# Performance work log

Hardware: AMD Instinct MI355X
Metric: run time of the kernel (lower is better)

## Reference

```python
import jax, jax.numpy as jnp
import numpy as np
from jax import lax

STRIDE = 4
RADII = (0.1, 0.2)
NSAMPLES = (16, 32)


def fps(xyz, npoint):
    """Iterative farthest point sampling. xyz: (B,N,3) -> idx (B,npoint) int32."""
    B, N, _ = xyz.shape

    def body(carry, _):
        dists, last = carry  # (B,N), (B,)
        last_pt = jnp.take_along_axis(xyz, last[:, None, None], axis=1)  # (B,1,3)
        d = jnp.sum((xyz - last_pt) ** 2, axis=-1)  # (B,N)
        dists = jnp.minimum(dists, d)
        nxt = jnp.argmax(dists, axis=-1).astype(jnp.int32)
        return (dists, nxt), last

    init = (jnp.full((B, N), 1e10, xyz.dtype), jnp.zeros((B,), jnp.int32))
    _, idxs = lax.scan(body, init, None, length=npoint)
    return jnp.transpose(idxs)  # (B, npoint)


def ball_query(radius, nsample, support_xyz, query_xyz):
    """First-nsample-in-ball neighbor indices, padded with the first valid index.
    Returns idx (B,S,K) int32."""
    N = support_xyz.shape[1]
    d2 = (jnp.sum(query_xyz ** 2, -1, keepdims=True)
          + jnp.sum(support_xyz ** 2, -1)[:, None, :]
          - 2.0 * jnp.einsum('bsd,bnd->bsn', query_xyz, support_xyz))  # (B,S,N)
    in_ball = d2 <= radius * radius
    key = jnp.where(in_ball, jnp.arange(N, dtype=jnp.int32), N)  # smallest index first
    neg_key, idx = lax.top_k(-key, nsample)  # smallest keys
    valid = (-neg_key) < N
    idx = jnp.where(valid, idx, idx[..., :1])  # pad empty slots with first neighbor
    return idx


def gather_points(pts, idx):
    """pts (B,N,D), idx (B,S,K) -> (B,S,K,D)"""
    B, S, K = idx.shape
    D = pts.shape[-1]
    out = jnp.take_along_axis(pts, idx.reshape(B, S * K, 1), axis=1)
    return out.reshape(B, S, K, D)


def scale_block(query_xyz, support_xyz, feats_t, radius, nsample, weights):
    idx = ball_query(radius, nsample, support_xyz, query_xyz)
    g_xyz = gather_points(support_xyz, idx) - query_xyz[:, :, None, :]  # relative coords
    g_feat = gather_points(feats_t, idx)
    h = jnp.concatenate([g_xyz, g_feat], axis=-1)  # (B,S,K,3+C)
    for W, b in weights:  # shared pointwise MLP (1x1 conv) + ReLU
        h = jax.nn.relu(jnp.einsum('bskc,cd->bskd', h, W) + b)
    return jnp.max(h, axis=2)  # max-pool over neighbors -> (B,S,Cout)


def setup_inputs() -> dict:
    key = jax.random.key(0)
    ks = jax.random.split(key, 10)
    B, N, C = 8, 8192, 64
    inp = {
        'support_xyz': jax.random.uniform(ks[0], (B, N, 3), jnp.float32),
        'support_features': jax.random.normal(ks[1], (B, C, N), jnp.float32),
    }
    dims0 = [(67, 64), (64, 64), (64, 128)]
    dims1 = [(67, 64), (64, 96), (96, 128)]
    k = 2
    for s, dims in ((0, dims0), (1, dims1)):
        for j, (din, dout) in enumerate(dims):
            inp[f's{s}_w{j}'] = jax.random.normal(ks[k], (din, dout), jnp.float32) * 0.02
            inp[f's{s}_b{j}'] = jnp.zeros((dout,), jnp.float32)
            k += 1
    return inp


def reference(support_xyz, support_features,
              s0_w0, s0_b0, s0_w1, s0_b1, s0_w2, s0_b2,
              s1_w0, s1_b0, s1_w1, s1_b1, s1_w2, s1_b2):
    B, N, _ = support_xyz.shape
    npoint = N // STRIDE
    idx = fps(support_xyz, npoint)  # (B,npoint)
    query_xyz = jnp.take_along_axis(support_xyz, idx[:, :, None], axis=1)  # (B,npoint,3)
    feats_t = jnp.transpose(support_features, (0, 2, 1))  # (B,N,C)
    w0 = [(s0_w0, s0_b0), (s0_w1, s0_b1), (s0_w2, s0_b2)]
    w1 = [(s1_w0, s1_b0), (s1_w1, s1_b1), (s1_w2, s1_b2)]
    f0 = scale_block(query_xyz, support_xyz, feats_t, RADII[0], NSAMPLES[0], w0)
    f1 = scale_block(query_xyz, support_xyz, feats_t, RADII[1], NSAMPLES[1], w1)
    new_features = jnp.transpose(jnp.concatenate([f0, f1], axis=-1), (0, 2, 1))  # (B,256,npoint)
    return query_xyz, new_features
```

## Files before the change

### kernel.cpp

```cpp
#include <hip/hip_runtime.h>

#define N_SUP 8192
#define N_QPT 2048
#define UNIT_LDS 41792
#define SMEM_BYTES 125440
#define N_CHUNKS 12288

typedef float v2f __attribute__((ext_vector_type(2)));

__device__ __forceinline__ float sumsq3(float x, float y, float z) {
#pragma clang fp contract(off)
  return x * x + y * y + z * z;
}

__device__ __forceinline__ float dot3(float ax, float ay, float az,
                                      float bx, float by, float bz) {
#pragma clang fp contract(off)
  return ax * bx + ay * by + az * bz;
}

__device__ __forceinline__ float d2_expand(float A, float Bn, float d) {
#pragma clang fp contract(off)
  return (A + Bn) - 2.0f * d;
}

template <int CTRL>
__device__ __forceinline__ unsigned long long dppmax64(unsigned long long k) {
  unsigned lo = (unsigned)k, hi = (unsigned)(k >> 32);
  unsigned olo =
      (unsigned)__builtin_amdgcn_update_dpp((int)lo, (int)lo, CTRL, 0xf, 0xf, false);
  unsigned ohi =
      (unsigned)__builtin_amdgcn_update_dpp((int)hi, (int)hi, CTRL, 0xf, 0xf, false);
  unsigned long long o = (((unsigned long long)ohi) << 32) | olo;
  return (o > k) ? o : k;
}

__device__ __forceinline__ unsigned long long wavemax_u64(unsigned long long k) {
  k = dppmax64<0x111>(k);
  k = dppmax64<0x112>(k);
  k = dppmax64<0x114>(k);
  k = dppmax64<0x118>(k);
  k = dppmax64<0x142>(k);
  k = dppmax64<0x143>(k);
  return k;
}

__global__ __launch_bounds__(256) void prep_xyz_kernel(
    const float* __restrict__ xyz, float* __restrict__ xs,
    float* __restrict__ ys, float* __restrict__ zs, float* __restrict__ bsq,
    int* __restrict__ flags) {
  int p = blockIdx.x * 256 + threadIdx.x;
  float x = xyz[p * 3 + 0];
  float y = xyz[p * 3 + 1];
  float z = xyz[p * 3 + 2];
  xs[p] = x; ys[p] = y; zs[p] = z;
  bsq[p] = sumsq3(x, y, z);
  if (blockIdx.x == 0) {
    flags[threadIdx.x] = 0;
    if (threadIdx.x < 64) flags[256 + threadIdx.x] = 0;
  }
}

__global__ __launch_bounds__(256) void transpose_feats_kernel(
    const float* __restrict__ feats, float* __restrict__ fT) {
  __shared__ float tile[64][65];
  int b = blockIdx.x >> 7;
  int nb = (blockIdx.x & 127) << 6;
  int t = threadIdx.x;
#pragma unroll
  for (int i = 0; i < 16; ++i) {
    int e = i * 256 + t;
    int c = e >> 6, n = e & 63;
    tile[n][c] = feats[(b * 64 + c) * N_SUP + nb + n];
  }
  __syncthreads();
#pragma unroll
  for (int i = 0; i < 16; ++i) {
    int e = i * 256 + t;
    int n = e >> 6, c = e & 63;
    fT[(b * N_SUP + nb + n) * 64 + c] = tile[n][c];
  }
}

__device__ __forceinline__ void bq_wave4(int lane, const float* __restrict__ sx,
                                         const float* __restrict__ sy,
                                         const float* __restrict__ sz,
                                         const float* __restrict__ sq,
                                         float qx, float qy, float qz,
                                         float r2, int K,
                                         int* __restrict__ out) {
  const float A = sumsq3(qx, qy, qz);
  int cnt = 0, first = 0;
  const unsigned long long lt = (1ull << lane) - 1ull;
  for (int base = 0; base < N_SUP; base += 256) {
    float4 x4 = ((const float4*)(sx + base))[lane];
    float4 y4 = ((const float4*)(sy + base))[lane];
    float4 z4 = ((const float4*)(sz + base))[lane];
    float4 q4 = ((const float4*)(sq + base))[lane];
    float da = d2_expand(A, q4.x, dot3(qx, qy, qz, x4.x, y4.x, z4.x));
    float db = d2_expand(A, q4.y, dot3(qx, qy, qz, x4.y, y4.y, z4.y));
    float dc = d2_expand(A, q4.z, dot3(qx, qy, qz, x4.z, y4.z, z4.z));
    float dd = d2_expand(A, q4.w, dot3(qx, qy, qz, x4.w, y4.w, z4.w));
    bool i0 = da <= r2, i1 = db <= r2, i2 = dc <= r2, i3 = dd <= r2;
    unsigned long long M0 = __ballot(i0), M1 = __ballot(i1);
    unsigned long long M2 = __ballot(i2), M3 = __ballot(i3);
    int below = __popcll(M0 & lt) + __popcll(M1 & lt) + __popcll(M2 & lt) +
                __popcll(M3 & lt);
    int p0 = cnt + below;
    int p1 = p0 + (i0 ? 1 : 0);
    int p2 = p1 + (i1 ? 1 : 0);
    int p3 = p2 + (i2 ? 1 : 0);
    int nb = base + 4 * lane;
    if (i0 && p0 < K) out[p0] = nb;
    if (i1 && p1 < K) out[p1] = nb + 1;
    if (i2 && p2 < K) out[p2] = nb + 2;
    if (i3 && p3 < K) out[p3] = nb + 3;
    if (cnt == 0) {
      unsigned mn = 0xFFFFFFFFu;
      if (M0) mn = min(mn, (unsigned)(4 * (__ffsll((long long)M0) - 1)));
      if (M1) mn = min(mn, (unsigned)(4 * (__ffsll((long long)M1) - 1) + 1));
      if (M2) mn = min(mn, (unsigned)(4 * (__ffsll((long long)M2) - 1) + 2));
      if (M3) mn = min(mn, (unsigned)(4 * (__ffsll((long long)M3) - 1) + 3));
      if (mn != 0xFFFFFFFFu) first = base + (int)mn;
    }
    cnt += __popcll(M0) + __popcll(M1) + __popcll(M2) + __popcll(M3);
    if (cnt >= K) break;
  }
  for (int p = cnt + lane; p < K; p += 64) out[p] = first;
}

template <int CIN, int SIN, int D, int SOUT>
__device__ __forceinline__ void dense_layer(const float* __restrict__ hin,
                                            float* __restrict__ hout,
                                            const float* __restrict__ W,
                                            const float* __restrict__ Bv,
                                            int w, int lane) {
  constexpr int CH = D / 16;
#pragma unroll
  for (int pass = 0; pass * 4 < CH; ++pass) {
    const int chunk = pass * 4 + w;
    if (chunk < CH) {
      const int co = chunk * 16;
      float acc[16];
#pragma unroll
      for (int j = 0; j < 16; ++j) acc[j] = Bv[co + j];
      const float* hr = hin + lane * SIN;
      const float* wp = W + co;
#pragma unroll 4
      for (int c = 0; c < CIN; ++c) {
        float a = hr[c];
#pragma unroll
        for (int j = 0; j < 16; ++j) acc[j] = fmaf(a, wp[c * D + j], acc[j]);
      }
      float* ho = hout + lane * SOUT + co;
#pragma unroll
      for (int j = 0; j < 16; ++j) ho[j] = fmaxf(acc[j], 0.0f);
    }
  }
}

template <int K, int Q, int C2, int S2, int CHOFF>
__device__ __forceinline__ void consumer_body(
    int tl, int qg0, float r2, char* um, const float* __restrict__ xs,
    const float* __restrict__ ys, const float* __restrict__ zs,
    const float* __restrict__ bsq, const float* __restrict__ fT, float* qxyz,
    int* prog, const float* __restrict__ W1, const float* __restrict__ B1,
    const float* __restrict__ W2, const float* __restrict__ B2,
    const float* __restrict__ W3, const float* __restrict__ B3,
    float* __restrict__ outf) {
  constexpr int S0 = 67, S1 = 65;
  float* smem = (float*)um;
  int* lidx = (int*)(um + 41472);
  float* qc = (float*)(um + 41728);
  float* h1 = smem;
  float* h0 = smem + 64 * S1;
  float* h2 = h0;
  const int w = __builtin_amdgcn_readfirstlane(tl >> 6);
  const int lane = tl & 63;
  const int b = qg0 >> 11;
  const int need = (qg0 & 2047) + Q;
  int* pp = prog + b * 32;
  while (__hip_atomic_load(pp, __ATOMIC_RELAXED, __HIP_MEMORY_SCOPE_AGENT) <
         need)
    __builtin_amdgcn_s_sleep(32);
  if (tl < Q * 3)
    qc[tl] = __hip_atomic_load(&qxyz[qg0 * 3 + tl], __ATOMIC_RELAXED,
                               __HIP_MEMORY_SCOPE_AGENT);
  __syncthreads();
  if (w < Q)
    bq_wave4(lane, xs + b * N_SUP, ys + b * N_SUP, zs + b * N_SUP,
             bsq + b * N_SUP, qc[w * 3], qc[w * 3 + 1], qc[w * 3 + 2], r2, K,
             lidx + w * K);
  __syncthreads();
  if (tl < 192) {
    int r = tl / 3, c2 = tl - r * 3;
    int qi = r / K;
    int n = lidx[r];
    const float* sp = (c2 == 0) ? xs : (c2 == 1) ? ys : zs;
    h0[r * S0 + c2] = sp[b * N_SUP + n] - qc[qi * 3 + c2];
  }
#pragma unroll
  for (int i = 0; i < 4; ++i) {
    int idx = tl + 256 * i;
    int r = idx >> 4, fi = idx & 15;
    int n = lidx[r];
    float4 v = ((const float4*)(fT + (size_t)(b * N_SUP + n) * 64))[fi];
    float* d = h0 + r * S0 + 3 + 4 * fi;
    d[0] = v.x; d[1] = v.y; d[2] = v.z; d[3] = v.w;
  }
  __syncthreads();
  dense_layer<67, S0, 64, S1>(h0, h1, W1, B1, w, lane);
  __syncthreads();
  dense_layer<64, S1, C2, S2>(h1, h2, W2, B2, w, lane);
  __syncthreads();
#pragma unroll
  for (int pass = 0; pass < 2; ++pass) {
    const int co = (pass * 4 + w) * 16;
    float acc[16];
#pragma unroll
    for (int j = 0; j < 16; ++j) acc[j] = B3[co + j];
    const float* hr = h2 + lane * S2;
#pragma unroll 4
    for (int c = 0; c < C2; ++c) {
      float a = hr[c];
#pragma unroll
      for (int j = 0; j < 16; ++j)
        acc[j] = fmaf(a, W3[c * 128 + co + j], acc[j]);
    }
#pragma unroll
    for (int j = 0; j < 16; ++j) acc[j] = fmaxf(acc[j], 0.0f);
#pragma unroll
    for (int off = K / 2; off >= 1; off >>= 1) {
#pragma unroll
      for (int j = 0; j < 16; ++j)
        acc[j] = fmaxf(acc[j], __shfl_xor(acc[j], off));
    }
    if ((lane & (K - 1)) == 0) {
      int qg = qg0 + (lane / K);
      int bo = qg >> 11, s = qg & 2047;
      float* dst = outf + ((bo * 256 + CHOFF + co) * 2048 + s);
#pragma unroll
      for (int j = 0; j < 16; ++j) dst[j * 2048] = acc[j];
    }
  }
}

__device__ void fps_producer(const float* __restrict__ xs,
                             const float* __restrict__ ys,
                             const float* __restrict__ zs, float* qxyz,
                             int* prog, char* smraw) {
  const int b = blockIdx.x;
  const int t = threadIdx.x;
  const bool act = t < 512;
  float* sxL = (float*)smraw;
  float* syL = (float*)(smraw + 32768);
  float* szL = (float*)(smraw + 65536);
  unsigned short* sorig = (unsigned short*)(smraw + 98304);
  unsigned* hist = (unsigned*)(smraw + 114688);
  unsigned* offs = (unsigned*)(smraw + 116736);
  unsigned* cursor = (unsigned*)(smraw + 118784);
  unsigned long long* skey = (unsigned long long*)(smraw + 120832);
  const float* bx = xs + b * N_SUP;
  const float* by = ys + b * N_SUP;
  const float* bz = zs + b * N_SUP;

  if (act) hist[t] = 0u;
  __syncthreads();
  if (act) {
    for (int j = 0; j < 16; ++j) {
      int n = t + j * 512;
      float x = bx[n], y = by[n], z = bz[n];
      int cx = min(7, (int)(x * 8.0f));
      int cy = min(7, (int)(y * 8.0f));
      int cz = min(7, (int)(z * 8.0f));
      atomicAdd(&hist[(cx << 6) | (cy << 3) | cz], 1u);
    }
  }
  __syncthreads();
  if (act) offs[t] = hist[t];
  __syncthreads();
  for (int d = 1; d < 512; d <<= 1) {
    unsigned v = 0;
    if (act && t >= d) v = offs[t - d];
    __syncthreads();
    if (act) offs[t] += v;
    __syncthreads();
  }
  if (act) cursor[t] = offs[t] - hist[t];
  __syncthreads();
  if (act) {
    for (int j = 0; j < 16; ++j) {
      int n = t + j * 512;
      float x = bx[n], y = by[n], z = bz[n];
      int cx = min(7, (int)(x * 8.0f));
      int cy = min(7, (int)(y * 8.0f));
      int cz = min(7, (int)(z * 8.0f));
      unsigned pos = atomicAdd(&cursor[(cx << 6) | (cy << 3) | cz], 1u);
      sxL[pos] = x; syL[pos] = y; szL[pos] = z;
      sorig[pos] = (unsigned short)n;
    }
  }
  __syncthreads();

  v2f px[8], py[8], pz[8], dm[8];
  unsigned payx[8], payy[8];
  float lox = 0, hix = 0, loy = 0, hiy = 0, loz = 0, hiz = 0;
  if (act) {
    const int base = t * 16;
#pragma unroll
    for (int j = 0; j < 8; ++j) {
      int p0 = base + 2 * j, p1 = p0 + 1;
      px[j] = (v2f){sxL[p0], sxL[p1]};
      py[j] = (v2f){syL[p0], syL[p1]};
      pz[j] = (v2f){szL[p0], szL[p1]};
      payx[j] = ((unsigned)(N_SUP - 1 - sorig[p0]) << 13) | (unsigned)p0;
      payy[j] = ((unsigned)(N_SUP - 1 - sorig[p1]) << 13) | (unsigned)p1;
      dm[j] = (v2f){1e10f, 1e10f};
    }
    lox = hix = px[0].x;
    loy = hiy = py[0].x;
    loz = hiz = pz[0].x;
#pragma unroll
    for (int j = 0; j < 8; ++j) {
      lox = fminf(lox, fminf(px[j].x, px[j].y));
      hix = fmaxf(hix, fmaxf(px[j].x, px[j].y));
      loy = fminf(loy, fminf(py[j].x, py[j].y));
      hiy = fmaxf(hiy, fmaxf(py[j].x, py[j].y));
      loz = fminf(loz, fminf(pz[j].x, pz[j].y));
      hiz = fmaxf(hiz, fmaxf(pz[j].x, pz[j].y));
    }
  }
  float tval = 1e10f;
  unsigned long long tkey = 0ull, wkey = 0ull;
  float lxp = bx[0], lyp = by[0], lzp = bz[0];
  float* q = qxyz + b * N_QPT * 3;
  if (t == 0) { q[0] = lxp; q[1] = lyp; q[2] = lzp; }
  const int wv = t >> 6;
  const bool is63 = ((t & 63) == 63) && act;

  for (int it = 1; it < N_QPT; ++it) {
    bool dirty = false;
    if (act) {
      float dxl = fmaxf(fmaxf(lox - lxp, lxp - hix), 0.0f);
      float dyl = fmaxf(fmaxf(loy - lyp, lyp - hiy), 0.0f);
      float dzl = fmaxf(fmaxf(loz - lzp, lzp - hiz), 0.0f);
      float db2 = dxl * dxl + dyl * dyl + dzl * dzl;
      dirty = db2 < tval * 1.0001f + 1e-12f;
    }
    if (__ballot(dirty)) {
      if (dirty) {
        float nx = -lxp, ny = -lyp, nz = -lzp;
        v2f nx2 = (v2f){nx, nx}, ny2 = (v2f){ny, ny}, nz2 = (v2f){nz, nz};
        float lm = -1.0f;
#pragma unroll
        for (int j = 0; j < 8; ++j) {
#pragma clang fp contract(off)
          v2f dx = px[j] + nx2;
          v2f dy = py[j] + ny2;
          v2f dz = pz[j] + nz2;
          v2f s = dx * dx + dy * dy;
          s = s + dz * dz;
          v2f nd = __builtin_elementwise_min(dm[j], s);
          dm[j] = nd;
          lm = fmaxf(lm, fmaxf(nd.x, nd.y));
        }
        tval = lm;
        unsigned pay = 0u;
#pragma unroll
        for (int j = 0; j < 8; ++j) {
          if (dm[j].x == tval) pay = max(pay, payx[j]);
          if (dm[j].y == tval) pay = max(pay, payy[j]);
        }
        tkey = (((unsigned long long)__float_as_uint(tval)) << 32) | pay;
      }
      wkey = wavemax_u64(tkey);
    }
    if (is63) skey[(it & 1) * 8 + wv] = wkey;
    __syncthreads();
    const ulonglong2* pk = (const ulonglong2*)(skey + (it & 1) * 8);
    ulonglong2 A = pk[0], B = pk[1], C = pk[2], D = pk[3];
    unsigned long long k0 = (A.y > A.x) ? A.y : A.x;
    unsigned long long k1 = (B.y > B.x) ? B.y : B.x;
    unsigned long long k2 = (C.y > C.x) ? C.y : C.x;
    unsigned long long k3 = (D.y > D.x) ? D.y : D.x;
    k0 = (k1 > k0) ? k1 : k0;
    k2 = (k3 > k2) ? k3 : k2;
    k0 = (k2 > k0) ? k2 : k0;
    unsigned pos = (unsigned)k0 & 0x1FFFu;
    lxp = sxL[pos]; lyp = syL[pos]; lzp = szL[pos];
    if (t == 0) {
      q[it * 3 + 0] = lxp;
      q[it * 3 + 1] = lyp;
      q[it * 3 + 2] = lzp;
      if ((it & 63) == 63)
        __hip_atomic_store(prog + b * 32, it + 1, __ATOMIC_RELEASE,
                           __HIP_MEMORY_SCOPE_AGENT);
    }
  }
  __syncthreads();
}

__global__ __launch_bounds__(768) void fused_kernel(
    const float* __restrict__ xs, const float* __restrict__ ys,
    const float* __restrict__ zs, const float* __restrict__ bsq,
    const float* __restrict__ fT, float* qxyz, float* outf, int* prog,
    int* qwork, const float* W10, const float* B10, const float* W11,
    const float* B11, const float* W12, const float* B12, const float* W20,
    const float* B20, const float* W21, const float* B21, const float* W22,
    const float* B22) {
  __shared__ __align__(16) char smraw[SMEM_BYTES];
  if (blockIdx.x < 8) {
    fps_producer(xs, ys, zs, qxyz, prog, smraw);
  }
  const int t = threadIdx.x;
  const int unit = t >> 8;
  const int tl = t & 255;
  char* um = smraw + unit * UNIT_LDS;
  int* lch = (int*)(smraw + 3 * UNIT_LDS);
  for (;;) {
    if (t == 0) {
      int c0 = atomicAdd(qwork, 3);
      lch[0] = c0;
      lch[1] = c0 + 1;
      lch[2] = c0 + 2;
    }
    __syncthreads();
    int c = lch[unit];
    if (lch[0] >= N_CHUNKS) return;
    if (c < N_CHUNKS) {
      int g = c / 3, r = c - g * 3;
      if (r == 0) {
        int qg0 = ((g & 7) << 11) + ((g >> 3) << 2);
        consumer_body<16, 4, 64, 65, 0>(tl, qg0, 0.01f, um, xs, ys, zs, bsq,
                                        fT, qxyz, prog, W10, B10, W11, B11,
                                        W12, B12, outf);
      } else {
        int h = 2 * g + r - 1;
        int qg0 = (((h >> 1) & 7) << 11) + ((h >> 4) << 2) + ((h & 1) << 1);
        consumer_body<32, 2, 96, 97, 128>(tl, qg0, 0.04f, um, xs, ys, zs, bsq,
                                          fT, qxyz, prog, W20, B20, W21, B21,
                                          W22, B22, outf);
      }
    } else {
      __syncthreads();
      __syncthreads();
      __syncthreads();
      __syncthreads();
      __syncthreads();
    }
  }
}

extern "C" void kernel_launch(void* const* d_in, const int* in_sizes, int n_in,
                              void* d_out, int out_size, void* d_ws,
                              size_t ws_size, hipStream_t stream) {
  const float* xyz = (const float*)d_in[0];
  const float* feats = (const float*)d_in[1];
  const float* wt[12];
  for (int i = 0; i < 12; ++i) wt[i] = (const float*)d_in[2 + i];

  float* ws = (float*)d_ws;
  float* xs = ws;
  float* ys = ws + 65536;
  float* zs = ws + 131072;
  float* bsq = ws + 196608;
  float* fT = ws + 262144;
  int* flags = (int*)(ws + 4456448);
  int* prog = flags;
  int* qwork = flags + 256;

  float* qxyz = (float*)d_out;
  float* outf = qxyz + 8 * 2048 * 3;

  prep_xyz_kernel<<<dim3(256), dim3(256), 0, stream>>>(xyz, xs, ys, zs, bsq,
                                                       flags);
  transpose_feats_kernel<<<dim3(1024), dim3(256), 0, stream>>>(feats, fT);
  fused_kernel<<<dim3(256), dim3(768), 0, stream>>>(
      xs, ys, zs, bsq, fT, qxyz, outf, prog, qwork, wt[0], wt[1], wt[2], wt[3],
      wt[4], wt[5], wt[6], wt[7], wt[8], wt[9], wt[10], wt[11]);
}
```

Before: 2.272 ms.

## Replace per-iteration FPS block barrier with tagged LDS slot spin-wait

The farthest-point-sampling producer used a __syncthreads every iteration to combine per-wave argmax keys. Each wave leader now publishes its key into LDS with an iteration tag stamped into unused bits, and every thread spins on relaxed atomic loads until all eight slots carry the current tag. Only the 512 active threads enter the producer, and producer blocks now return instead of joining the consumer work loop. The aim is to shorten the serial critical path of the 2048-iteration FPS loop by removing full-block barriers, at the cost of LDS polling traffic and losing the producer blocks' help with MLP work afterward.

```diff
diff --git a/kernel.cpp b/kernel.cpp
--- a/kernel.cpp
+++ b/kernel.cpp
@@ -245,13 +245,12 @@
   }
 }
 
-__device__ void fps_producer(const float* __restrict__ xs,
-                             const float* __restrict__ ys,
-                             const float* __restrict__ zs, float* qxyz,
-                             int* prog, char* smraw) {
+__device__ void fps_producer_bf(const float* __restrict__ xs,
+                                const float* __restrict__ ys,
+                                const float* __restrict__ zs, float* qxyz,
+                                int* prog, char* smraw) {
   const int b = blockIdx.x;
   const int t = threadIdx.x;
-  const bool act = t < 512;
   float* sxL = (float*)smraw;
   float* syL = (float*)(smraw + 32768);
   float* szL = (float*)(smraw + 65536);
@@ -259,76 +258,69 @@
   unsigned* hist = (unsigned*)(smraw + 114688);
   unsigned* offs = (unsigned*)(smraw + 116736);
   unsigned* cursor = (unsigned*)(smraw + 118784);
-  unsigned long long* skey = (unsigned long long*)(smraw + 120832);
+  unsigned long long* slots = (unsigned long long*)(smraw + 120832);
   const float* bx = xs + b * N_SUP;
   const float* by = ys + b * N_SUP;
   const float* bz = zs + b * N_SUP;
 
-  if (act) hist[t] = 0u;
-  __syncthreads();
-  if (act) {
-    for (int j = 0; j < 16; ++j) {
-      int n = t + j * 512;
-      float x = bx[n], y = by[n], z = bz[n];
-      int cx = min(7, (int)(x * 8.0f));
-      int cy = min(7, (int)(y * 8.0f));
-      int cz = min(7, (int)(z * 8.0f));
-      atomicAdd(&hist[(cx << 6) | (cy << 3) | cz], 1u);
-    }
-  }
-  __syncthreads();
-  if (act) offs[t] = hist[t];
+  hist[t] = 0u;
+  if (t < 16) slots[t] = 0ull;
+  __syncthreads();
+  for (int j = 0; j < 16; ++j) {
+    int n = t + j * 512;
+    float x = bx[n], y = by[n], z = bz[n];
+    int cx = min(7, (int)(x * 8.0f));
+    int cy = min(7, (int)(y * 8.0f));
+    int cz = min(7, (int)(z * 8.0f));
+    atomicAdd(&hist[(cx << 6) | (cy << 3) | cz], 1u);
+  }
+  __syncthreads();
+  offs[t] = hist[t];
   __syncthreads();
   for (int d = 1; d < 512; d <<= 1) {
-    unsigned v = 0;
-    if (act && t >= d) v = offs[t - d];
+    unsigned v = (t >= d) ? offs[t - d] : 0u;
     __syncthreads();
-    if (act) offs[t] += v;
+    offs[t] += v;
     __syncthreads();
   }
-  if (act) cursor[t] = offs[t] - hist[t];
-  __syncthreads();
-  if (act) {
-    for (int j = 0; j < 16; ++j) {
-      int n = t + j * 512;
-      float x = bx[n], y = by[n], z = bz[n];
-      int cx = min(7, (int)(x * 8.0f));
-      int cy = min(7, (int)(y * 8.0f));
-      int cz = min(7, (int)(z * 8.0f));
-      unsigned pos = atomicAdd(&cursor[(cx << 6) | (cy << 3) | cz], 1u);
-      sxL[pos] = x; syL[pos] = y; szL[pos] = z;
-      sorig[pos] = (unsigned short)n;
-    }
+  cursor[t] = offs[t] - hist[t];
+  __syncthreads();
+  for (int j = 0; j < 16; ++j) {
+    int n = t + j * 512;
+    float x = bx[n], y = by[n], z = bz[n];
+    int cx = min(7, (int)(x * 8.0f));
+    int cy = min(7, (int)(y * 8.0f));
+    int cz = min(7, (int)(z * 8.0f));
+    unsigned pos = atomicAdd(&cursor[(cx << 6) | (cy << 3) | cz], 1u);
+    sxL[pos] = x; syL[pos] = y; szL[pos] = z;
+    sorig[pos] = (unsigned short)n;
   }
   __syncthreads();
 
   v2f px[8], py[8], pz[8], dm[8];
   unsigned payx[8], payy[8];
-  float lox = 0, hix = 0, loy = 0, hiy = 0, loz = 0, hiz = 0;
-  if (act) {
-    const int base = t * 16;
-#pragma unroll
-    for (int j = 0; j < 8; ++j) {
-      int p0 = base + 2 * j, p1 = p0 + 1;
-      px[j] = (v2f){sxL[p0], sxL[p1]};
-      py[j] = (v2f){syL[p0], syL[p1]};
-      pz[j] = (v2f){szL[p0], szL[p1]};
-      payx[j] = ((unsigned)(N_SUP - 1 - sorig[p0]) << 13) | (unsigned)p0;
-      payy[j] = ((unsigned)(N_SUP - 1 - sorig[p1]) << 13) | (unsigned)p1;
-      dm[j] = (v2f){1e10f, 1e10f};
-    }
-    lox = hix = px[0].x;
-    loy = hiy = py[0].x;
-    loz = hiz = pz[0].x;
-#pragma unroll
-    for (int j = 0; j < 8; ++j) {
-      lox = fminf(lox, fminf(px[j].x, px[j].y));
-      hix = fmaxf(hix, fmaxf(px[j].x, px[j].y));
-      loy = fminf(loy, fminf(py[j].x, py[j].y));
-      hiy = fmaxf(hiy, fmaxf(py[j].x, py[j].y));
-      loz = fminf(loz, fminf(pz[j].x, pz[j].y));
-      hiz = fmaxf(hiz, fmaxf(pz[j].x, pz[j].y));
-    }
+  const int base = t * 16;
+#pragma unroll
+  for (int j = 0; j < 8; ++j) {
+    int p0 = base + 2 * j, p1 = p0 + 1;
+    px[j] = (v2f){sxL[p0], sxL[p1]};
+    py[j] = (v2f){syL[p0], syL[p1]};
+    pz[j] = (v2f){szL[p0], szL[p1]};
+    payx[j] = ((unsigned)(N_SUP - 1 - sorig[p0]) << 13) | (unsigned)p0;
+    payy[j] = ((unsigned)(N_SUP - 1 - sorig[p1]) << 13) | (unsigned)p1;
+    dm[j] = (v2f){1e10f, 1e10f};
+  }
+  float lox = px[0].x, hix = px[0].x;
+  float loy = py[0].x, hiy = py[0].x;
+  float loz = pz[0].x, hiz = pz[0].x;
+#pragma unroll
+  for (int j = 0; j < 8; ++j) {
+    lox = fminf(lox, fminf(px[j].x, px[j].y));
+    hix = fmaxf(hix, fmaxf(px[j].x, px[j].y));
+    loy = fminf(loy, fminf(py[j].x, py[j].y));
+    hiy = fmaxf(hiy, fmaxf(py[j].x, py[j].y));
+    loz = fminf(loz, fminf(pz[j].x, pz[j].y));
+    hiz = fmaxf(hiz, fmaxf(pz[j].x, pz[j].y));
   }
   float tval = 1e10f;
   unsigned long long tkey = 0ull, wkey = 0ull;
@@ -336,17 +328,16 @@
   float* q = qxyz + b * N_QPT * 3;
   if (t == 0) { q[0] = lxp; q[1] = lyp; q[2] = lzp; }
   const int wv = t >> 6;
-  const bool is63 = ((t & 63) == 63) && act;
+  const bool is63 = (t & 63) == 63;
+  const unsigned long long tagm = 0x3Full << 26;
+  __syncthreads();
 
   for (int it = 1; it < N_QPT; ++it) {
-    bool dirty = false;
-    if (act) {
-      float dxl = fmaxf(fmaxf(lox - lxp, lxp - hix), 0.0f);
-      float dyl = fmaxf(fmaxf(loy - lyp, lyp - hiy), 0.0f);
-      float dzl = fmaxf(fmaxf(loz - lzp, lzp - hiz), 0.0f);
-      float db2 = dxl * dxl + dyl * dyl + dzl * dzl;
-      dirty = db2 < tval * 1.0001f + 1e-12f;
-    }
+    float dxl = fmaxf(fmaxf(lox - lxp, lxp - hix), 0.0f);
+    float dyl = fmaxf(fmaxf(loy - lyp, lyp - hiy), 0.0f);
+    float dzl = fmaxf(fmaxf(loz - lzp, lzp - hiz), 0.0f);
+    float db2 = dxl * dxl + dyl * dyl + dzl * dzl;
+    bool dirty = db2 < tval * 1.0001f + 1e-12f;
     if (__ballot(dirty)) {
       if (dirty) {
         float nx = -lxp, ny = -lyp, nz = -lzp;
@@ -375,18 +366,45 @@
       }
       wkey = wavemax_u64(tkey);
     }
-    if (is63) skey[(it & 1) * 8 + wv] = wkey;
-    __syncthreads();
-    const ulonglong2* pk = (const ulonglong2*)(skey + (it & 1) * 8);
-    ulonglong2 A = pk[0], B = pk[1], C = pk[2], D = pk[3];
-    unsigned long long k0 = (A.y > A.x) ? A.y : A.x;
-    unsigned long long k1 = (B.y > B.x) ? B.y : B.x;
-    unsigned long long k2 = (C.y > C.x) ? C.y : C.x;
-    unsigned long long k3 = (D.y > D.x) ? D.y : D.x;
-    k0 = (k1 > k0) ? k1 : k0;
-    k2 = (k3 > k2) ? k3 : k2;
-    k0 = (k2 > k0) ? k2 : k0;
-    unsigned pos = (unsigned)k0 & 0x1FFFu;
+    const unsigned long long tagv = ((unsigned long long)(it & 63)) << 26;
+    unsigned long long* sp = slots + (it & 1) * 8;
+    if (is63)
+      __hip_atomic_store(&sp[wv], wkey | tagv, __ATOMIC_RELAXED,
+                         __HIP_MEMORY_SCOPE_WORKGROUP);
+    unsigned long long kmax;
+    for (;;) {
+      unsigned long long k0 = __hip_atomic_load(&sp[0], __ATOMIC_RELAXED,
+                                                __HIP_MEMORY_SCOPE_WORKGROUP);
+      unsigned long long k1 = __hip_atomic_load(&sp[1], __ATOMIC_RELAXED,
+                                                __HIP_MEMORY_SCOPE_WORKGROUP);
+      unsigned long long k2 = __hip_atomic_load(&sp[2], __ATOMIC_RELAXED,
+                                                __HIP_MEMORY_SCOPE_WORKGROUP);
+      unsigned long long k3 = __hip_atomic_load(&sp[3], __ATOMIC_RELAXED,
+                                                __HIP_MEMORY_SCOPE_WORKGROUP);
+      unsigned long long k4 = __hip_atomic_load(&sp[4], __ATOMIC_RELAXED,
+                                                __HIP_MEMORY_SCOPE_WORKGROUP);
+      unsigned long long k5 = __hip_atomic_load(&sp[5], __ATOMIC_RELAXED,
+                                                __HIP_MEMORY_SCOPE_WORKGROUP);
+      unsigned long long k6 = __hip_atomic_load(&sp[6], __ATOMIC_RELAXED,
+                                                __HIP_MEMORY_SCOPE_WORKGROUP);
+      unsigned long long k7 = __hip_atomic_load(&sp[7], __ATOMIC_RELAXED,
+                                                __HIP_MEMORY_SCOPE_WORKGROUP);
+      unsigned long long bad = ((k0 & tagm) ^ tagv) | ((k1 & tagm) ^ tagv) |
+                               ((k2 & tagm) ^ tagv) | ((k3 & tagm) ^ tagv) |
+                               ((k4 & tagm) ^ tagv) | ((k5 & tagm) ^ tagv) |
+                               ((k6 & tagm) ^ tagv) | ((k7 & tagm) ^ tagv);
+      if (bad == 0ull) {
+        k0 = (k1 > k0) ? k1 : k0;
+        k2 = (k3 > k2) ? k3 : k2;
+        k4 = (k5 > k4) ? k5 : k4;
+        k6 = (k7 > k6) ? k7 : k6;
+        k0 = (k2 > k0) ? k2 : k0;
+        k4 = (k6 > k4) ? k6 : k4;
+        kmax = (k4 > k0) ? k4 : k0;
+        break;
+      }
+    }
+    unsigned pos = (unsigned)kmax & 0x1FFFu;
     lxp = sxL[pos]; lyp = syL[pos]; lzp = szL[pos];
     if (t == 0) {
       q[it * 3 + 0] = lxp;
@@ -397,7 +415,6 @@
                            __HIP_MEMORY_SCOPE_AGENT);
     }
   }
-  __syncthreads();
 }
 
 __global__ __launch_bounds__(768) void fused_kernel(
@@ -410,7 +427,8 @@
     const float* B22) {
   __shared__ __align__(16) char smraw[SMEM_BYTES];
   if (blockIdx.x < 8) {
-    fps_producer(xs, ys, zs, qxyz, prog, smraw);
+    if (threadIdx.x < 512) fps_producer_bf(xs, ys, zs, qxyz, prog, smraw);
+    return;
   }
   const int t = threadIdx.x;
   const int unit = t >> 8;
```

Result: no change. 2.294 ms (+1.0%).
